# Kernel optimization log

Measured on AMD Instinct MI355X. Metric: run time of the kernel, lower is better.

## Reference

```python
import jax, jax.numpy as jnp
import numpy as np

B, T, H, V = 256, 256, 512, 32000
L = 3  # stacked LSTM layers


def setup_inputs() -> dict:
    key = jax.random.key(0)
    ks = jax.random.split(key, 12)
    s = 0.05
    n = lambda k, shp: (jax.random.normal(k, shp, jnp.float32) * s)
    return {
        "text_1": jax.random.randint(ks[0], (B, T), 0, V, dtype=jnp.int32),
        "text_2": jax.random.randint(ks[1], (B, T), 0, V, dtype=jnp.int32),
        "text_3": jax.random.randint(ks[2], (B, T), 0, V, dtype=jnp.int32),
        "emb": n(ks[3], (V, H)),
        "Wx": n(ks[4], (L, H, 4 * H)),
        "Wh": n(ks[5], (L, H, 4 * H)),
        "b": jnp.zeros((L, 4 * H), jnp.float32),
        "g1": jnp.ones((3 * H,), jnp.float32), "beta1": jnp.zeros((3 * H,), jnp.float32),
        "W1": n(ks[6], (3 * H, 2 * H)), "bd1": jnp.zeros((2 * H,), jnp.float32),
        "g2": jnp.ones((2 * H,), jnp.float32), "beta2": jnp.zeros((2 * H,), jnp.float32),
        "W2": n(ks[7], (2 * H, H // 5)), "bd2": jnp.zeros((H // 5,), jnp.float32),
        "g3": jnp.ones((H // 5,), jnp.float32), "beta3": jnp.zeros((H // 5,), jnp.float32),
        "W3": n(ks[8], (H // 5, 4)), "bd3": jnp.zeros((4,), jnp.float32),
    }


def _lstm_stack(tokens, emb, Wx, Wh, b):
    # tokens: [B, T] int -> last hidden of top layer [B, H]
    x = emb[tokens]                      # [B, T, H]
    x = jnp.transpose(x, (1, 0, 2))      # [T, B, H] (scan over time)
    bsz, h = x.shape[1], Wh.shape[1]
    for l in range(Wx.shape[0]):
        Wx_l, Wh_l, b_l = Wx[l], Wh[l], b[l]
        def step(carry, xt):
            hprev, cprev = carry
            gates = xt @ Wx_l + hprev @ Wh_l + b_l      # [B, 4H]
            i, f, g, o = jnp.split(gates, 4, axis=-1)
            c = jax.nn.sigmoid(f) * cprev + jax.nn.sigmoid(i) * jnp.tanh(g)
            hnew = jax.nn.sigmoid(o) * jnp.tanh(c)
            return (hnew, c), hnew
        init = (jnp.zeros((bsz, h), x.dtype), jnp.zeros((bsz, h), x.dtype))
        _, x = jax.lax.scan(step, init, x)
    return x[-1]                          # rnn_output[:, -1, :]


def _bn(x, gamma, beta, eps=1e-3):
    m = jnp.mean(x, axis=0)
    v = jnp.var(x, axis=0)
    return gamma * (x - m) * jax.lax.rsqrt(v + eps) + beta


def reference(text_1, text_2, text_3, emb, Wx, Wh, b,
              g1, beta1, W1, bd1, g2, beta2, W2, bd2, g3, beta3, W3, bd3):
    r1 = _lstm_stack(text_1, emb, Wx, Wh, b)
    r2 = _lstm_stack(text_2, emb, Wx, Wh, b)
    r3 = _lstm_stack(text_3, emb, Wx, Wh, b)
    r = jnp.concatenate([r1, r2, r3], axis=1)   # [B, 3H]
    r = _bn(r, g1, beta1)
    r = jax.nn.selu(r @ W1 + bd1)
    r = _bn(r, g2, beta2)
    r = jax.nn.selu(r @ W2 + bd2)
    r = _bn(r, g3, beta3)
    return r @ W3 + bd3                          # [B, 4] logits
```

## Files before the change

### kernel.cpp

```cpp
#include <hip/hip_runtime.h>
#include <hip/hip_bf16.h>

typedef __attribute__((ext_vector_type(8))) short short8;
typedef __attribute__((ext_vector_type(4))) float floatx4;
typedef __attribute__((ext_vector_type(4))) unsigned uintx4;

namespace {
constexpr int kB1 = 256;
constexpr int kT  = 256;
constexpr int kH  = 512;
constexpr int kL  = 3;
constexpr int kB3 = 768;
constexpr int kK  = 1024;
constexpr int kN  = 2048;
constexpr int kV  = 32000;
constexpr size_t kHB = (size_t)kB3 * kH;
constexpr int kRing = 16;
constexpr int kFenceP = 12;

constexpr size_t WREP_OFF   = 0;
constexpr size_t WREP_BYTES = (size_t)kL * kK * kN * 2;
constexpr size_t BREP_OFF   = WREP_OFF + WREP_BYTES;
constexpr size_t BREP_BYTES = (size_t)kL * kN * 4;
constexpr size_t EMB_OFF    = BREP_OFF + BREP_BYTES;
constexpr size_t EMB_BYTES  = (size_t)kV * kH * 2;
constexpr size_t HBUF_OFF   = EMB_OFF + EMB_BYTES;
constexpr size_t HBUF_BYTES = (size_t)kL * kRing * kHB * 2;
constexpr size_t CBUF_OFF   = HBUF_OFF + HBUF_BYTES;
constexpr size_t CBUF_BYTES = (size_t)kL * kHB * 4;
constexpr size_t BNA_OFF    = CBUF_OFF + CBUF_BYTES;
constexpr size_t BNC_OFF    = BNA_OFF + 1536 * 4;
constexpr size_t Z1_OFF     = BNC_OFF + 1536 * 4;
constexpr size_t Z2_OFF     = Z1_OFF + (size_t)256 * 1024 * 4;
constexpr size_t FLAG_OFF   = Z2_OFF + (size_t)256 * 102 * 4;
constexpr size_t BAR_OFF    = FLAG_OFF + 128;
constexpr size_t WS_NEEDED  = BAR_OFF + 4096;
constexpr int kPersistGrid  = 192;
constexpr int kGenIdx       = 960;
}

__device__ __forceinline__ float ldf(const void* p, size_t idx, int isf32) {
  if (isf32) return ((const float*)p)[idx];
  return __bfloat162float(((const __hip_bfloat16*)p)[idx]);
}

__device__ __forceinline__ short f2bs(float x) {
  union { __hip_bfloat16 h; short s; } u;
  u.h = __float2bfloat16(x);
  return u.s;
}

__device__ __forceinline__ short8 cvt8(const float* q) {
  float4 lo = *(const float4*)q;
  float4 hi = *(const float4*)(q + 4);
  short8 v;
  v[0] = f2bs(lo.x); v[1] = f2bs(lo.y); v[2] = f2bs(lo.z); v[3] = f2bs(lo.w);
  v[4] = f2bs(hi.x); v[5] = f2bs(hi.y); v[6] = f2bs(hi.z); v[7] = f2bs(hi.w);
  return v;
}

__global__ void detect_kernel(const unsigned* __restrict__ g1, int* __restrict__ flag,
                              unsigned* __restrict__ bar) {
  int tid = threadIdx.x;
#pragma unroll
  for (int i = 0; i < 4; i++)
    __hip_atomic_store(&bar[tid + 256 * i], 0u, __ATOMIC_RELAXED, __HIP_MEMORY_SCOPE_AGENT);
  if (tid == 0 && blockIdx.x == 0)
    *flag = (g1[0] == 0x3F800000u) ? 1 : 0;
}

__global__ __launch_bounds__(256) void repack_kernel(
    const void* __restrict__ Wx, const void* __restrict__ Wh,
    const void* __restrict__ bias, const int* __restrict__ flagp,
    __hip_bfloat16* __restrict__ Wrep, float* __restrict__ brep) {
  int isf32 = *flagp;
  int idx = blockIdx.x * 256 + threadIdx.x;
  if (idx >= kL * kK * kN) return;
  int j  = idx & 7;
  int n2 = (idx >> 3) & (kN - 1);
  int kg = (idx >> 14) & 127;
  int l  = idx >> 21;
  int k  = kg * 8 + j;
  int ntile = n2 >> 7, c = n2 & 127, g = c >> 5, ul = c & 31;
  int u = ntile * 32 + ul;
  int col = g * 512 + u;
  float v;
  if (k < kH) v = ldf(Wx, ((size_t)l * kH + k) * kN + col, isf32);
  else        v = ldf(Wh, ((size_t)l * kH + (k - kH)) * kN + col, isf32);
  Wrep[idx] = __float2bfloat16(v);
  if (kg == 0 && j == 0) brep[l * kN + n2] = ldf(bias, (size_t)l * kN + col, isf32);
}

__global__ __launch_bounds__(256) void embrep_kernel(
    const void* __restrict__ emb, const int* __restrict__ flagp,
    __hip_bfloat16* __restrict__ er) {
  int isf32 = *flagp;
  size_t base = ((size_t)blockIdx.x * 256 + threadIdx.x) * 8;
  if (base >= (size_t)kV * kH) return;
  if (isf32) *(short8*)(er + base) = cvt8((const float*)emb + base);
  else       *(short8*)(er + base) = *(const short8*)((const __hip_bfloat16*)emb + base);
}

__device__ __forceinline__ void grid_barrier(unsigned* bar, int bid, int tid,
                                             unsigned sval, bool fence) {
  __syncthreads();
  if (tid == 0)
    __hip_atomic_store(&bar[bid], sval, __ATOMIC_RELEASE, __HIP_MEMORY_SCOPE_AGENT);
  if (bid == 0) {
    if (tid < 64) {
      const unsigned* fp = bar + ((tid < 48) ? (tid << 2) : 0);
      long long t0 = (long long)__builtin_amdgcn_s_memrealtime();
      int it = 0;
      for (;;) {
        uintx4 a;
        asm volatile("global_load_dwordx4 %0, %1, off sc0 sc1\n\t"
                     "s_waitcnt vmcnt(0)"
                     : "=v"(a) : "v"(fp));
        bool ok = a[0] == sval && a[1] == sval && a[2] == sval && a[3] == sval;
        if (__all(ok)) break;
        __builtin_amdgcn_s_sleep(1);
        if (((++it) & 15) == 0 &&
            (long long)__builtin_amdgcn_s_memrealtime() - t0 > 20000000LL) break;
      }
      if (tid == 0)
        __hip_atomic_store(&bar[kGenIdx], sval, __ATOMIC_RELEASE, __HIP_MEMORY_SCOPE_AGENT);
    }
  } else if (tid == 0) {
    long long t0 = (long long)__builtin_amdgcn_s_memrealtime();
    int it = 0;
    while (__hip_atomic_load(&bar[kGenIdx], __ATOMIC_RELAXED, __HIP_MEMORY_SCOPE_AGENT) < sval) {
      __builtin_amdgcn_s_sleep(4);
      if (((++it) & 63) == 0 &&
          (long long)__builtin_amdgcn_s_memrealtime() - t0 > 20000000LL) break;
    }
  }
  __syncthreads();
  if (fence)
    __builtin_amdgcn_fence(__ATOMIC_ACQUIRE, "agent");
}

__global__ __launch_bounds__(1024) void persist_kernel(
    const __hip_bfloat16* __restrict__ Wrep, const float* __restrict__ brep,
    __hip_bfloat16* __restrict__ hbuf, const __hip_bfloat16* __restrict__ er,
    const int* __restrict__ flagp, const int* __restrict__ t1,
    const int* __restrict__ t2, const int* __restrict__ t3,
    unsigned* __restrict__ bar) {
  __shared__ __align__(16) char smem[24576 + 4 * 96 * 66 * 4];
  float* gl = (float*)(smem + 24576);

  const int tid = threadIdx.x;
  const int bid = blockIdx.x;
  const int xcd = bid & 7;
  const int j_  = bid >> 3;
  const int l   = j_ >> 3;
  const int r_  = j_ & 7;
  const int c_  = (xcd + 5 * l) & 7;
  const int mt  = (c_ >> 2) * 4 + (r_ & 3);
  const int nt  = (c_ & 3) * 2 + (r_ >> 2);
  const int rot = (r_ >> 2) * 8;

  const int wv = tid >> 6, lane = tid & 63, lm = lane & 15, lq = lane >> 4;
  const int mrow = (wv >> 3) * 48;
  const int ncol = nt * 256 + (wv & 7) * 32;

  const int r0 = tid >> 3;
  const int c8 = tid & 7;
  const bool stg = (tid < 768);
  const int R  = mt * 96 + r0;
  const unsigned ro = (unsigned)R * kH + c8 * 8;

  const int* tb = nullptr;
  int tk = 0;
  if (l == 0 && stg) {
    tb = (((R >> 8) == 0) ? t1 : ((R >> 8) == 1) ? t2 : t3) + (R & 255) * kT;
    tk = tb[0];
  }

  const __hip_bfloat16* WB = Wrep + (size_t)l * kK * kN;
  const float bv0 = brep[l * kN + ncol + lm];
  const float bv1 = brep[l * kN + ncol + 16 + lm];

  char* aw = smem + r0 * 128 + ((c8 ^ (r0 & 7)) << 4);
  int oswz[2];
#pragma unroll
  for (int kk = 0; kk < 2; kk++) oswz[kk] = (((kk * 4 + lq) ^ (lm & 7)) << 4);

  const int cuu = tid & 63, crb = tid >> 6;
  float creg[6] = {0.f, 0.f, 0.f, 0.f, 0.f, 0.f};

  short8 aCur, aNxt;
  short8 bA[2][2], bB[2][2];
  const __hip_bfloat16* xe = nullptr;
  if (l == 0 && stg) xe = er + (size_t)tk * kH + c8 * 8;

#pragma unroll 1
  for (int s = 0; s < kT + kL - 1; s++) {
    const int t = s - l;
    if (t >= 0 && t < kT) {
      const __hip_bfloat16* hp = hbuf + ((size_t)l * kRing + ((t + kRing - 1) & (kRing - 1))) * kHB;
      const __hip_bfloat16* xh = nullptr;
      int nk = 0;
      if (l == 0) {
        if (stg && t + 1 < kT) nk = tb[t + 1];
      } else {
        xh = hbuf + ((size_t)(l - 1) * kRing + (t & (kRing - 1))) * kHB;
      }

      auto loadA = [&](int p, short8& d) {
        if (!stg) return;
        if (p < 8) {
          if (l == 0) d = *(const short8*)(xe + p * 64);
          else        d = *(const short8*)(xh + ro + p * 64);
        } else if (t == 0) {
          short8 z = {0, 0, 0, 0, 0, 0, 0, 0};
          d = z;
        } else {
          d = *(const short8*)(hp + ro + (p - 8) * 64);
        }
      };
      auto loadB = [&](int p, short8 (&bf)[2][2]) {
#pragma unroll
        for (int kk = 0; kk < 2; kk++)
#pragma unroll
          for (int nf = 0; nf < 2; nf++) {
            int kg = p * 8 + kk * 4 + lq;
            bf[kk][nf] = *(const short8*)(WB + ((size_t)kg * kN + ncol + nf * 16 + lm) * 8);
          }
      };

      if (t == 0 || l != 0 || rot >= 8) loadA(rot, aCur);
      if (t == 0) loadB(rot, bA);

      floatx4 zf = {0.f, 0.f, 0.f, 0.f};
      floatx4 acc[3][2];
#pragma unroll
      for (int a = 0; a < 3; a++) { acc[a][0] = zf; acc[a][1] = zf; }

#pragma unroll
      for (int si = 0; si < 16; si++) {
        const int buf = si & 1;
        if (stg) *(short8*)(aw + buf * 12288) = aCur;
        __syncthreads();
        if (si < 15) {
          const int pn = (si + 1 + rot) & 15;
          loadA(pn, aNxt);
          if (buf == 0) loadB(pn, bB); else loadB(pn, bA);
        }
        const char* arb = smem + buf * 12288 + lm * 128;
#pragma unroll
        for (int kk = 0; kk < 2; kk++) {
          const short8* bf = buf ? &bB[kk][0] : &bA[kk][0];
          short8 af0 = *(const short8*)(arb + (mrow + 0) * 128 + oswz[kk]);
          short8 af1 = *(const short8*)(arb + (mrow + 16) * 128 + oswz[kk]);
          short8 af2 = *(const short8*)(arb + (mrow + 32) * 128 + oswz[kk]);
          acc[0][0] = __builtin_amdgcn_mfma_f32_16x16x32_bf16(af0, bf[0], acc[0][0], 0, 0, 0);
          acc[0][1] = __builtin_amdgcn_mfma_f32_16x16x32_bf16(af0, bf[1], acc[0][1], 0, 0, 0);
          acc[1][0] = __builtin_amdgcn_mfma_f32_16x16x32_bf16(af1, bf[0], acc[1][0], 0, 0, 0);
          acc[1][1] = __builtin_amdgcn_mfma_f32_16x16x32_bf16(af1, bf[1], acc[1][1], 0, 0, 0);
          acc[2][0] = __builtin_amdgcn_mfma_f32_16x16x32_bf16(af2, bf[0], acc[2][0], 0, 0, 0);
          acc[2][1] = __builtin_amdgcn_mfma_f32_16x16x32_bf16(af2, bf[1], acc[2][1], 0, 0, 0);
        }
        aCur = aNxt;
        if (buf) {
        }
      }

#pragma unroll
      for (int mf = 0; mf < 3; mf++)
#pragma unroll
        for (int nf = 0; nf < 2; nf++)
#pragma unroll
          for (int r = 0; r < 4; r++) {
            int rowf = mrow + mf * 16 + lq * 4 + r;
            int ct = (wv & 7) * 32 + nf * 16 + lm;
            int ut = ct >> 7, cc = ct & 127;
            int g = cc >> 5, ul = ut * 32 + (cc & 31);
            gl[((size_t)g * 96 + rowf) * 66 + ul] = acc[mf][nf][r] + (nf ? bv1 : bv0);
          }
      __syncthreads();

      __hip_bfloat16* hout = hbuf + ((size_t)l * kRing + (t & (kRing - 1))) * kHB;
#pragma unroll
      for (int ii = 0; ii < 6; ii++) {
        int rowf = crb + 16 * ii;
        float gi = fminf(fmaxf(gl[(0 * 96 + rowf) * 66 + cuu], -40.f), 40.f);
        float gf = fminf(fmaxf(gl[(1 * 96 + rowf) * 66 + cuu], -40.f), 40.f);
        float gg = fminf(fmaxf(gl[(2 * 96 + rowf) * 66 + cuu], -40.f), 40.f);
        float go = fminf(fmaxf(gl[(3 * 96 + rowf) * 66 + cuu], -40.f), 40.f);
        float c_old = (t > 0) ? creg[ii] : 0.f;
        float si = 1.f / (1.f + __expf(-gi));
        float sf = 1.f / (1.f + __expf(-gf));
        float so = 1.f / (1.f + __expf(-go));
        float cn = sf * c_old + si * tanhf(gg);
        float hn = so * tanhf(cn);
        creg[ii] = cn;
        union { __hip_bfloat16 h; unsigned short u; } cv;
        cv.h = __float2bfloat16(hn);
        __hip_atomic_store(
            (unsigned short*)(hout + (size_t)(mt * 96 + rowf) * kH + nt * 64 + cuu),
            cv.u, __ATOMIC_RELAXED, __HIP_MEMORY_SCOPE_AGENT);
      }

      if (t + 1 < kT) {
        loadB(rot, bA);
        if (l == 0 && stg) {
          tk = nk;
          xe = er + (size_t)tk * kH + c8 * 8;
          if (rot < 8) loadA(rot, aCur);
        }
      }
    }
    if (s < kT + kL - 2)
      grid_barrier(bar, bid, tid, (unsigned)(s + 1), (s % kFenceP) == (kFenceP - 1));
  }
}

__global__ __launch_bounds__(256) void step_kernel(
    int s,
    const __hip_bfloat16* __restrict__ Wrep, const float* __restrict__ brep,
    __hip_bfloat16* __restrict__ hbuf, float* __restrict__ cbuf,
    const void* __restrict__ emb, const int* __restrict__ flagp,
    const int* __restrict__ t1, const int* __restrict__ t2, const int* __restrict__ t3) {
  __shared__ __align__(16) char smem[34816];

  int bid = blockIdx.x;
  int l  = bid / 192;
  int rr = bid % 192;
  int nt = rr & 15;
  int mt = rr >> 4;
  int t = s - l;
  if (t < 0 || t >= kT) return;

  int isf32 = *flagp;
  int tid = threadIdx.x;
  int wv = tid >> 6, lane = tid & 63;
  int lm = lane & 15, lq = lane >> 4;

  int arow = tid >> 2;
  int kc   = tid & 3;
  int row_g = mt * 64 + arow;

  const void* xsrc;
  bool xf32 = false;
  if (l == 0) {
    int i = row_g >> 8, bb = row_g & 255;
    const int* txt = (i == 0) ? t1 : (i == 1) ? t2 : t3;
    int tok = txt[bb * kT + t];
    if (isf32) { xsrc = (const void*)((const float*)emb + (size_t)tok * kH); xf32 = true; }
    else         xsrc = (const void*)((const __hip_bfloat16*)emb + (size_t)tok * kH);
  } else {
    const __hip_bfloat16* hIn = hbuf + ((size_t)(l - 1) * kRing + (t & (kRing - 1))) * kHB;
    xsrc = (const void*)(hIn + (size_t)row_g * kH);
  }
  const __hip_bfloat16* hrow = nullptr;
  if (t > 0) {
    const __hip_bfloat16* hPrev = hbuf + ((size_t)l * kRing + ((t + kRing - 1) & (kRing - 1))) * kHB;
    hrow = hPrev + (size_t)row_g * kH;
  }

  floatx4 zf = {0.f, 0.f, 0.f, 0.f};
  floatx4 acc[4][2];
#pragma unroll
  for (int a = 0; a < 4; a++)
#pragma unroll
    for (int b = 0; b < 2; b++) acc[a][b] = zf;

  const __hip_bfloat16* WB = Wrep + (size_t)l * kK * kN;
  int n0w = nt * 128 + wv * 32;

#pragma unroll 1
  for (int sl = 0; sl < 8; sl++) {
    short8 bfrag[4][2];
#pragma unroll
    for (int kk = 0; kk < 4; kk++)
#pragma unroll
      for (int nf = 0; nf < 2; nf++) {
        size_t kg = (size_t)(sl * 16 + kk * 4 + lq);
        const __hip_bfloat16* p = WB + (kg * kN + (n0w + nf * 16 + lm)) * 8;
        bfrag[kk][nf] = *(const short8*)p;
      }
    short8 av[4];
    bool zero = (sl >= 4) && (t == 0);
    if (!zero) {
      if (sl < 4 && xf32) {
        const float* sf = (const float*)xsrc + sl * 128;
#pragma unroll
        for (int jj = 0; jj < 4; jj++) {
          const float* q = sf + kc * 8 + jj * 32;
          float4 lo = *(const float4*)q;
          float4 hi = *(const float4*)(q + 4);
          short8 v;
          v[0] = f2bs(lo.x); v[1] = f2bs(lo.y); v[2] = f2bs(lo.z); v[3] = f2bs(lo.w);
          v[4] = f2bs(hi.x); v[5] = f2bs(hi.y); v[6] = f2bs(hi.z); v[7] = f2bs(hi.w);
          av[jj] = v;
        }
      } else {
        const __hip_bfloat16* src = (sl < 4)
            ? ((const __hip_bfloat16*)xsrc + sl * 128)
            : (hrow + (sl - 4) * 128);
#pragma unroll
        for (int jj = 0; jj < 4; jj++)
          av[jj] = *(const short8*)(src + kc * 8 + jj * 32);
      }
    } else {
      short8 vz = {0, 0, 0, 0, 0, 0, 0, 0};
#pragma unroll
      for (int jj = 0; jj < 4; jj++) av[jj] = vz;
    }
    __syncthreads();
#pragma unroll
    for (int jj = 0; jj < 4; jj++) {
      int klocal = kc * 8 + jj * 32;
      *(short8*)(smem + arow * 272 + klocal * 2) = av[jj];
    }
    __syncthreads();
#pragma unroll
    for (int kk = 0; kk < 4; kk++) {
      short8 afrag[4];
#pragma unroll
      for (int mf = 0; mf < 4; mf++) {
        int rowf = mf * 16 + lm;
        afrag[mf] = *(const short8*)(smem + rowf * 272 + kk * 64 + lq * 16);
      }
#pragma unroll
      for (int mf = 0; mf < 4; mf++)
#pragma unroll
        for (int nf = 0; nf < 2; nf++)
          acc[mf][nf] = __builtin_amdgcn_mfma_f32_16x16x32_bf16(
              afrag[mf], bfrag[kk][nf], acc[mf][nf], 0, 0, 0);
    }
  }

  const float* bl = brep + l * kN;
#pragma unroll
  for (int nf = 0; nf < 2; nf++) {
    float bv = bl[n0w + nf * 16 + lm];
#pragma unroll
    for (int mf = 0; mf < 4; mf++)
#pragma unroll
      for (int r = 0; r < 4; r++) acc[mf][nf][r] += bv;
  }

  __syncthreads();
  float* gl = (float*)smem;
#pragma unroll
  for (int mf = 0; mf < 4; mf++)
#pragma unroll
    for (int nf = 0; nf < 2; nf++)
#pragma unroll
      for (int r = 0; r < 4; r++) {
        int rowf = mf * 16 + lq * 4 + r;
        int uu   = nf * 16 + lm;
        gl[((size_t)wv * 64 + rowf) * 34 + uu] = acc[mf][nf][r];
      }
  __syncthreads();

  float* cl = cbuf + (size_t)l * kHB;
  __hip_bfloat16* hout = hbuf + ((size_t)l * kRing + (t & (kRing - 1))) * kHB;
#pragma unroll
  for (int ii = 0; ii < 8; ii++) {
    int idx = tid + 256 * ii;
    int uu = idx & 31, rowf = idx >> 5;
    float gi = fminf(fmaxf(gl[(0 * 64 + rowf) * 34 + uu], -40.f), 40.f);
    float gf = fminf(fmaxf(gl[(1 * 64 + rowf) * 34 + uu], -40.f), 40.f);
    float gg = fminf(fmaxf(gl[(2 * 64 + rowf) * 34 + uu], -40.f), 40.f);
    float go = fminf(fmaxf(gl[(3 * 64 + rowf) * 34 + uu], -40.f), 40.f);
    int bg = mt * 64 + rowf;
    int ug = nt * 32 + uu;
    size_t off = (size_t)bg * kH + ug;
    float c_old = (t > 0) ? cl[off] : 0.f;
    float si = 1.f / (1.f + __expf(-gi));
    float sf = 1.f / (1.f + __expf(-gf));
    float so = 1.f / (1.f + __expf(-go));
    float cn = sf * c_old + si * tanhf(gg);
    float hn = so * tanhf(cn);
    cl[off] = cn;
    hout[off] = __float2bfloat16(hn);
  }
}

__global__ __launch_bounds__(256) void stats_kernel(
    int ncols, int mode, const void* __restrict__ src,
    const void* __restrict__ gamma, const void* __restrict__ beta,
    const int* __restrict__ flagp, float* __restrict__ bn_a, float* __restrict__ bn_c) {
  int isf32 = *flagp;
  int col = blockIdx.x * 256 + threadIdx.x;
  if (col >= ncols) return;
  float sum = 0.f, ss = 0.f;
  for (int b = 0; b < kB1; b++) {
    float v;
    if (mode == 0) {
      const __hip_bfloat16* h = (const __hip_bfloat16*)src;
      v = __bfloat162float(h[((size_t)((col >> 9) * kB1 + b)) * kH + (col & 511)]);
    } else {
      v = ((const float*)src)[(size_t)b * ncols + col];
    }
    v = fmaxf(-1e15f, fminf(v, 1e15f));
    sum += v; ss += v * v;
  }
  float mean = sum * (1.f / kB1);
  float var  = ss * (1.f / kB1) - mean * mean;
  float a = ldf(gamma, col, isf32) * rsqrtf(var + 1e-3f);
  bn_a[col] = a;
  bn_c[col] = ldf(beta, col, isf32) - mean * a;
}

__global__ __launch_bounds__(256) void headgemm_kernel(
    int Kd, int Nd, int mode, const void* __restrict__ Asrc,
    const float* __restrict__ bn_a, const float* __restrict__ bn_c,
    const void* __restrict__ W, const void* __restrict__ bias,
    const int* __restrict__ flagp, float* __restrict__ out, int do_selu) {
  __shared__ float As[32][65];
  __shared__ float Bs[32][65];
  int isf32 = *flagp;
  int tid = threadIdx.x;
  int bx = blockIdx.x, by = blockIdx.y;
  int tx = tid & 15, ty = tid >> 4;
  float acc[4][4] = {};
  int am = tid & 63, ak = tid >> 6;
  int bk = tid >> 3, bn8 = (tid & 7) * 8;
  for (int ks = 0; ks < Kd; ks += 32) {
    __syncthreads();
    for (int jj = 0; jj < 8; jj++) {
      int kl = ak * 8 + jj;
      int kg = ks + kl;
      int mg = by * 64 + am;
      float v;
      if (mode == 0) {
        const __hip_bfloat16* h = (const __hip_bfloat16*)Asrc;
        v = __bfloat162float(h[((size_t)((kg >> 9) * kB1 + mg)) * kH + (kg & 511)]);
      } else {
        v = ((const float*)Asrc)[(size_t)mg * Kd + kg];
      }
      As[kl][am] = v * bn_a[kg] + bn_c[kg];
    }
    for (int e = 0; e < 8; e++) {
      int col = bx * 64 + bn8 + e;
      Bs[bk][bn8 + e] = (col < Nd) ? ldf(W, (size_t)(ks + bk) * Nd + col, isf32) : 0.f;
    }
    __syncthreads();
    for (int k = 0; k < 32; k++) {
      float ar[4], br[4];
#pragma unroll
      for (int i = 0; i < 4; i++) ar[i] = As[k][ty * 4 + i];
#pragma unroll
      for (int j = 0; j < 4; j++) br[j] = Bs[k][tx * 4 + j];
#pragma unroll
      for (int i = 0; i < 4; i++)
#pragma unroll
        for (int j = 0; j < 4; j++) acc[i][j] += ar[i] * br[j];
    }
  }
  for (int i = 0; i < 4; i++) {
    int row = by * 64 + ty * 4 + i;
    for (int j = 0; j < 4; j++) {
      int col = bx * 64 + tx * 4 + j;
      if (col < Nd) {
        float y = acc[i][j] + ldf(bias, col, isf32);
        if (do_selu)
          y = (y > 0.f) ? 1.0507009873554805f * y
                        : 1.0507009873554805f * 1.6732632423543772f * (__expf(y) - 1.f);
        out[(size_t)row * Nd + col] = y;
      }
    }
  }
}

__global__ __launch_bounds__(256) void final_kernel(
    const float* __restrict__ z2, const float* __restrict__ bn_a, const float* __restrict__ bn_c,
    const void* __restrict__ W3, const void* __restrict__ bd3,
    const int* __restrict__ flagp, void* __restrict__ out) {
  int isf32 = *flagp;
  int b = threadIdx.x;
  float acc[4] = {0.f, 0.f, 0.f, 0.f};
  for (int j = 0; j < 102; j++) {
    float y = z2[b * 102 + j] * bn_a[j] + bn_c[j];
#pragma unroll
    for (int g = 0; g < 4; g++) acc[g] += y * ldf(W3, j * 4 + g, isf32);
  }
#pragma unroll
  for (int g = 0; g < 4; g++) {
    float y = acc[g] + ldf(bd3, g, isf32);
    if (isf32) ((float*)out)[b * 4 + g] = y;
    else ((__hip_bfloat16*)out)[b * 4 + g] = __float2bfloat16(y);
  }
}

extern "C" void kernel_launch(void* const* d_in, const int* in_sizes, int n_in,
                              void* d_out, int out_size, void* d_ws, size_t ws_size,
                              hipStream_t stream) {
  const int* t1 = (const int*)d_in[0];
  const int* t2 = (const int*)d_in[1];
  const int* t3 = (const int*)d_in[2];
  const void* emb = d_in[3];
  const void* Wx  = d_in[4];
  const void* Wh  = d_in[5];
  const void* bb  = d_in[6];
  const void* g1  = d_in[7];
  const void* be1 = d_in[8];
  const void* W1  = d_in[9];
  const void* bd1 = d_in[10];
  const void* g2  = d_in[11];
  const void* be2 = d_in[12];
  const void* W2  = d_in[13];
  const void* bd2 = d_in[14];
  const void* g3  = d_in[15];
  const void* be3 = d_in[16];
  const void* W3  = d_in[17];
  const void* bd3 = d_in[18];

  char* ws = (char*)d_ws;
  __hip_bfloat16* Wrep = (__hip_bfloat16*)(ws + WREP_OFF);
  float* brep = (float*)(ws + BREP_OFF);
  __hip_bfloat16* embrep = (__hip_bfloat16*)(ws + EMB_OFF);
  __hip_bfloat16* hbuf = (__hip_bfloat16*)(ws + HBUF_OFF);
  float* cbuf = (float*)(ws + CBUF_OFF);
  float* bn_a = (float*)(ws + BNA_OFF);
  float* bn_c = (float*)(ws + BNC_OFF);
  float* z1 = (float*)(ws + Z1_OFF);
  float* z2 = (float*)(ws + Z2_OFF);
  int* flag = (int*)(ws + FLAG_OFF);
  unsigned* bar = (unsigned*)(ws + BAR_OFF);

  static int persist_ok = -1;
  if (persist_ok < 0) {
    int nb = 0, ncu = 0, dev = 0;
    (void)hipGetDevice(&dev);
    (void)hipDeviceGetAttribute(&ncu, hipDeviceAttributeMultiprocessorCount, dev);
    hipError_t e = hipOccupancyMaxActiveBlocksPerMultiprocessor(&nb, persist_kernel, 1024, 0);
    persist_ok = (e == hipSuccess && (long)nb * (long)ncu >= kPersistGrid &&
                  ws_size >= WS_NEEDED) ? 1 : 0;
  }

  detect_kernel<<<1, 256, 0, stream>>>((const unsigned*)g1, flag, bar);

  repack_kernel<<<(kL * kK * kN) / 256, 256, 0, stream>>>(Wx, Wh, bb, flag, Wrep, brep);
  embrep_kernel<<<(kV * kH) / (256 * 8), 256, 0, stream>>>(emb, flag, embrep);

  if (persist_ok) {
    persist_kernel<<<kPersistGrid, 1024, 0, stream>>>(
        Wrep, brep, hbuf, embrep, flag, t1, t2, t3, bar);
  } else {
    for (int s = 0; s < kT + kL - 1; s++)
      step_kernel<<<3 * 192, 256, 0, stream>>>(s, Wrep, brep, hbuf, cbuf, emb, flag, t1, t2, t3);
  }

  const __hip_bfloat16* hTop = hbuf + (size_t)(2 * kRing + ((kT - 1) & (kRing - 1))) * kHB;
  stats_kernel<<<6, 256, 0, stream>>>(1536, 0, hTop, g1, be1, flag, bn_a, bn_c);
  headgemm_kernel<<<dim3(16, 4), 256, 0, stream>>>(1536, 1024, 0, hTop, bn_a, bn_c, W1, bd1, flag, z1, 1);
  stats_kernel<<<4, 256, 0, stream>>>(1024, 1, z1, g2, be2, flag, bn_a, bn_c);
  headgemm_kernel<<<dim3(2, 4), 256, 0, stream>>>(1024, 102, 1, z1, bn_a, bn_c, W2, bd2, flag, z2, 1);
  stats_kernel<<<1, 256, 0, stream>>>(102, 1, z2, g3, be3, flag, bn_a, bn_c);
  final_kernel<<<1, 256, 0, stream>>>(z2, bn_a, bn_c, W3, bd3, flag, (void*)d_out);
}
```

Before: 6.062 ms.

## Replace global grid barrier with per-tile dependency flags in persistent LSTM kernel

```diff
diff --git a/kernel.cpp b/kernel.cpp
--- a/kernel.cpp
+++ b/kernel.cpp
@@ -3,7 +3,6 @@
 
 typedef __attribute__((ext_vector_type(8))) short short8;
 typedef __attribute__((ext_vector_type(4))) float floatx4;
-typedef __attribute__((ext_vector_type(4))) unsigned uintx4;
 
 namespace {
 constexpr int kB1 = 256;
@@ -36,7 +35,6 @@
 constexpr size_t BAR_OFF    = FLAG_OFF + 128;
 constexpr size_t WS_NEEDED  = BAR_OFF + 4096;
 constexpr int kPersistGrid  = 192;
-constexpr int kGenIdx       = 960;
 }
 
 __device__ __forceinline__ float ldf(const void* p, size_t idx, int isf32) {
@@ -101,42 +99,19 @@
   else       *(short8*)(er + base) = *(const short8*)((const __hip_bfloat16*)emb + base);
 }
 
-__device__ __forceinline__ void grid_barrier(unsigned* bar, int bid, int tid,
-                                             unsigned sval, bool fence) {
-  __syncthreads();
-  if (tid == 0)
-    __hip_atomic_store(&bar[bid], sval, __ATOMIC_RELEASE, __HIP_MEMORY_SCOPE_AGENT);
-  if (bid == 0) {
-    if (tid < 64) {
-      const unsigned* fp = bar + ((tid < 48) ? (tid << 2) : 0);
-      long long t0 = (long long)__builtin_amdgcn_s_memrealtime();
-      int it = 0;
-      for (;;) {
-        uintx4 a;
-        asm volatile("global_load_dwordx4 %0, %1, off sc0 sc1\n\t"
-                     "s_waitcnt vmcnt(0)"
-                     : "=v"(a) : "v"(fp));
-        bool ok = a[0] == sval && a[1] == sval && a[2] == sval && a[3] == sval;
-        if (__all(ok)) break;
-        __builtin_amdgcn_s_sleep(1);
-        if (((++it) & 15) == 0 &&
-            (long long)__builtin_amdgcn_s_memrealtime() - t0 > 20000000LL) break;
-      }
-      if (tid == 0)
-        __hip_atomic_store(&bar[kGenIdx], sval, __ATOMIC_RELEASE, __HIP_MEMORY_SCOPE_AGENT);
-    }
-  } else if (tid == 0) {
-    long long t0 = (long long)__builtin_amdgcn_s_memrealtime();
-    int it = 0;
-    while (__hip_atomic_load(&bar[kGenIdx], __ATOMIC_RELAXED, __HIP_MEMORY_SCOPE_AGENT) < sval) {
-      __builtin_amdgcn_s_sleep(4);
-      if (((++it) & 63) == 0 &&
-          (long long)__builtin_amdgcn_s_memrealtime() - t0 > 20000000LL) break;
-    }
-  }
-  __syncthreads();
-  if (fence)
-    __builtin_amdgcn_fence(__ATOMIC_ACQUIRE, "agent");
+__device__ __forceinline__ void wait8(const unsigned* fp, unsigned target) {
+  const int lane = threadIdx.x & 7;
+  long long t0 = (long long)__builtin_amdgcn_s_memrealtime();
+  int it = 0;
+  for (;;) {
+    unsigned v;
+    asm volatile("global_load_dword %0, %1, off sc0 sc1\n\ts_waitcnt vmcnt(0)"
+                 : "=v"(v) : "v"(fp + lane));
+    if (__all(v >= target)) break;
+    __builtin_amdgcn_s_sleep(1);
+    if (((++it) & 31) == 0 &&
+        (long long)__builtin_amdgcn_s_memrealtime() - t0 > 20000000LL) break;
+  }
 }
 
 __global__ __launch_bounds__(1024) void persist_kernel(
@@ -156,12 +131,19 @@
   const int r_  = j_ & 7;
   const int c_  = (xcd + 5 * l) & 7;
   const int mt  = (c_ >> 2) * 4 + (r_ & 3);
-  const int nt  = (c_ & 3) * 2 + (r_ >> 2);
-  const int rot = (r_ >> 2) * 8;
+  const int nt  = (c_ & 3) * 2 + (r_ >> 4 ? 0 : (r_ >> 2));
+  const int nt2 = (c_ & 3) * 2 + (r_ >> 2);
+  const int ntF = nt2;
+
+  unsigned* prod = bar;
+  unsigned* myflag = prod + ((l * 8 + mt) * 8 + ntF);
+  const unsigned* grpSelf  = prod + (l * 8 + mt) * 8;
+  const unsigned* grpBelow = (l > 0) ? prod + ((l - 1) * 8 + mt) * 8 : nullptr;
+  const unsigned* grpAbove = (l < 2) ? prod + ((l + 1) * 8 + mt) * 8 : nullptr;
 
   const int wv = tid >> 6, lane = tid & 63, lm = lane & 15, lq = lane >> 4;
   const int mrow = (wv >> 3) * 48;
-  const int ncol = nt * 256 + (wv & 7) * 32;
+  const int ncol = ntF * 256 + (wv & 7) * 32;
 
   const int r0 = tid >> 3;
   const int c8 = tid & 7;
@@ -196,7 +178,8 @@
 #pragma unroll 1
   for (int s = 0; s < kT + kL - 1; s++) {
     const int t = s - l;
-    if (t >= 0 && t < kT) {
+    if (t >= kT) break;
+    if (t >= 0) {
       const __hip_bfloat16* hp = hbuf + ((size_t)l * kRing + ((t + kRing - 1) & (kRing - 1))) * kHB;
       const __hip_bfloat16* xh = nullptr;
       int nk = 0;
@@ -228,8 +211,9 @@
           }
       };
 
-      if (t == 0 || l != 0 || rot >= 8) loadA(rot, aCur);
-      if (t == 0) loadB(rot, bA);
+      if (l > 0) wait8(grpBelow, (unsigned)(t + 1));
+      if (l != 0 || t == 0) loadA(0, aCur);
+      if (t == 0) loadB(0, bA);
 
       floatx4 zf = {0.f, 0.f, 0.f, 0.f};
       floatx4 acc[3][2];
@@ -242,9 +226,9 @@
         if (stg) *(short8*)(aw + buf * 12288) = aCur;
         __syncthreads();
         if (si < 15) {
-          const int pn = (si + 1 + rot) & 15;
-          loadA(pn, aNxt);
-          if (buf == 0) loadB(pn, bB); else loadB(pn, bA);
+          if (si == 7 && t > 0) wait8(grpSelf, (unsigned)t);
+          loadA(si + 1, aNxt);
+          if (buf == 0) loadB(si + 1, bB); else loadB(si + 1, bA);
         }
         const char* arb = smem + buf * 12288 + lm * 128;
 #pragma unroll
@@ -261,8 +245,6 @@
           acc[2][1] = __builtin_amdgcn_mfma_f32_16x16x32_bf16(af2, bf[1], acc[2][1], 0, 0, 0);
         }
         aCur = aNxt;
-        if (buf) {
-        }
       }
 
 #pragma unroll
@@ -278,6 +260,8 @@
             gl[((size_t)g * 96 + rowf) * 66 + ul] = acc[mf][nf][r] + (nf ? bv1 : bv0);
           }
       __syncthreads();
+
+      if (l < 2 && t >= kRing) wait8(grpAbove, (unsigned)(t - (kRing - 1)));
 
       __hip_bfloat16* hout = hbuf + ((size_t)l * kRing + (t & (kRing - 1))) * kHB;
 #pragma unroll
@@ -297,22 +281,28 @@
         union { __hip_bfloat16 h; unsigned short u; } cv;
         cv.h = __float2bfloat16(hn);
         __hip_atomic_store(
-            (unsigned short*)(hout + (size_t)(mt * 96 + rowf) * kH + nt * 64 + cuu),
+            (unsigned short*)(hout + (size_t)(mt * 96 + rowf) * kH + ntF * 64 + cuu),
             cv.u, __ATOMIC_RELAXED, __HIP_MEMORY_SCOPE_AGENT);
       }
 
+      __syncthreads();
+      if (tid == 0)
+        __hip_atomic_store(myflag, (unsigned)(t + 1), __ATOMIC_RELEASE,
+                           __HIP_MEMORY_SCOPE_AGENT);
+
       if (t + 1 < kT) {
-        loadB(rot, bA);
+        loadB(0, bA);
         if (l == 0 && stg) {
           tk = nk;
           xe = er + (size_t)tk * kH + c8 * 8;
-          if (rot < 8) loadA(rot, aCur);
+          loadA(0, aCur);
         }
       }
     }
-    if (s < kT + kL - 2)
-      grid_barrier(bar, bid, tid, (unsigned)(s + 1), (s % kFenceP) == (kFenceP - 1));
-  }
+    if (s < kT + kL - 2 && (s % kFenceP) == (kFenceP - 1))
+      __builtin_amdgcn_fence(__ATOMIC_ACQUIRE, "agent");
+  }
+  (void)nt;
 }
 
 __global__ __launch_bounds__(256) void step_kernel(
```

New measurement: 6.012 ms. Within noise of the previous version (-0.8%).
